# Kernel tuning notes

Measured on AMD Instinct MI355X. Metric: run time of the kernel, lower is better.

Reference implementation:

```python
import jax, jax.numpy as jnp
import numpy as np

DIM = 2048
N_HEADS = 16
KV_RANK = 512
NOPE = 128
ROPE = 64
VDIM = 128
QK_HEAD = NOPE + ROPE  # 192
THETA = 10000.0
EPS = 1e-6
SCALE = QK_HEAD ** -0.5  # mscale == 1.0
NEG_INF = -1e30


def precompute_freqs(seq_len, head_dim, theta=THETA):
    # cos/sin of position*freq, shape (seq_len, head_dim//2)
    freqs = 1.0 / theta ** (np.arange(0, head_dim, 2, dtype=np.float32) / head_dim)
    ang = np.outer(np.arange(seq_len, dtype=np.float32), freqs)
    return jnp.asarray(np.cos(ang)), jnp.asarray(np.sin(ang))


def apply_rope(x, cos, sin):
    # x: (B, S, H, r); cos/sin: (S, r//2). Complex rotation on (even, odd) pairs.
    x2 = x.reshape(*x.shape[:-1], -1, 2)
    x0, x1 = x2[..., 0], x2[..., 1]
    c = cos[None, :, None, :]
    s = sin[None, :, None, :]
    r0 = x0 * c - x1 * s
    r1 = x0 * s + x1 * c
    return jnp.stack([r0, r1], axis=-1).reshape(x.shape)


def rmsnorm(x, w, eps=EPS):
    rms = jnp.sqrt(jnp.mean(x * x, axis=-1, keepdims=True) + eps)
    return x / rms * w


def setup_inputs() -> dict:
    key = jax.random.key(0)
    ks = jax.random.split(key, 5)
    B, S = 2, 2048
    sc = lambda n: 1.0 / np.sqrt(n)
    return {
        "x": jax.random.normal(ks[0], (B, S, DIM), jnp.float32),
        "wq": jax.random.normal(ks[1], (N_HEADS * QK_HEAD, DIM), jnp.float32) * sc(DIM),
        "wkv_a": jax.random.normal(ks[2], (KV_RANK + ROPE, DIM), jnp.float32) * sc(DIM),
        "wkv_b": jax.random.normal(ks[3], (N_HEADS * (NOPE + VDIM), KV_RANK), jnp.float32) * sc(KV_RANK),
        "wo": jax.random.normal(ks[4], (DIM, N_HEADS * VDIM), jnp.float32) * sc(N_HEADS * VDIM),
        "kv_norm_w": jnp.ones((KV_RANK,), jnp.float32),
    }


def reference(x, wq, wkv_a, wkv_b, wo, kv_norm_w):
    # SimpleMLA forward, attn_impl='absorb', start_pos=0 (prefill, causal mask)
    B, S, _ = x.shape
    cos, sin = precompute_freqs(S, ROPE)

    # Q projection (q_lora_rank == 0 -> full rank)
    q = (x @ wq.T).reshape(B, S, N_HEADS, QK_HEAD)
    q_nope, q_pe = q[..., :NOPE], q[..., NOPE:]
    q_pe = apply_rope(q_pe, cos, sin)  # (B,S,H,ROPE)

    # KV-A projection -> latent kv + shared positional key
    kv = x @ wkv_a.T  # (B,S,KV_RANK+ROPE)
    kv_lat, k_pe = kv[..., :KV_RANK], kv[..., KV_RANK:]
    k_pe = apply_rope(k_pe[:, :, None, :], cos, sin)[:, :, 0, :]  # (B,S,ROPE)

    # Absorb: fold wkv_b's nope-half into q; kv_cache is the normalized latent
    wkv_b_h = wkv_b.reshape(N_HEADS, NOPE + VDIM, KV_RANK)
    q_lat = jnp.einsum("bshd,hdc->bshc", q_nope, wkv_b_h[:, :NOPE])  # (B,S,H,C)
    kv_cache = rmsnorm(kv_lat, kv_norm_w)  # (B,T,C)

    scores = (jnp.einsum("bshc,btc->bsht", q_lat, kv_cache)
              + jnp.einsum("bshr,btr->bsht", q_pe, k_pe)) * SCALE
    causal = jnp.tril(jnp.ones((S, S), bool))  # (s, t)
    scores = jnp.where(causal[None, :, None, :], scores, NEG_INF)
    attn = jax.nn.softmax(scores, axis=-1)  # (B,S,H,T)

    out_lat = jnp.einsum("bsht,btc->bshc", attn, kv_cache)  # (B,S,H,C)
    out = jnp.einsum("bshc,hdc->bshd", out_lat, wkv_b_h[:, NOPE:])  # (B,S,H,VDIM)
    return out.reshape(B, S, N_HEADS * VDIM) @ wo.T
```

## Files before the change

kernel.cpp:

```cpp
#include <hip/hip_runtime.h>

typedef unsigned short u16;
typedef unsigned int u32;
typedef __attribute__((ext_vector_type(4))) short short4_t;
typedef __attribute__((ext_vector_type(8))) short short8_t;
typedef __attribute__((ext_vector_type(4))) float f32x4;
typedef __attribute__((ext_vector_type(2))) float f32x2;
typedef __attribute__((ext_vector_type(2))) unsigned int uint2v;
typedef __attribute__((ext_vector_type(8))) __bf16 bf16x8;

#define NH 16
#define SLEN 2048
#define NB 2
#define NTOK 4096
#define SCALE_F 0.07216878364870323f

__device__ __forceinline__ u16 f2bf(float f) {
  unsigned u = __builtin_bit_cast(unsigned, f);
  unsigned r = (u + 0x7FFFu + ((u >> 16) & 1u)) >> 16;
  return (u16)r;
}
__device__ __forceinline__ float bf2f(u16 v) {
  unsigned u = ((unsigned)v) << 16;
  return __builtin_bit_cast(float, u);
}
__device__ __forceinline__ f32x4 mfma16(short8_t a, short8_t b, f32x4 c) {
  return __builtin_amdgcn_mfma_f32_16x16x32_bf16(
      __builtin_bit_cast(bf16x8, a), __builtin_bit_cast(bf16x8, b), c, 0, 0, 0);
}
__device__ __forceinline__ void async16(const u16* g, u16* l) {
  __builtin_amdgcn_global_load_lds(
      (const __attribute__((address_space(1))) unsigned int*)g,
      (__attribute__((address_space(3))) unsigned int*)l, 16, 0, 0);
}

__global__ __launch_bounds__(256) void conv_bf16(const float* __restrict__ in,
                                                 u16* __restrict__ out, int n4) {
  int i = blockIdx.x * 256 + threadIdx.x;
  int stride = gridDim.x * 256;
  for (; i < n4; i += stride) {
    f32x4 v = ((const f32x4*)in)[i];
    short4_t s = {(short)f2bf(v[0]), (short)f2bf(v[1]), (short)f2bf(v[2]),
                  (short)f2bf(v[3])};
    ((short4_t*)out)[i] = s;
  }
}

__global__ void rope_tables(float* __restrict__ cost, float* __restrict__ sint) {
  int s = blockIdx.x, i = threadIdx.x;
  double freq = pow(10000.0, -(double)(2 * i) / 64.0);
  double ang = (double)s * freq;
  cost[s * 32 + i] = (float)cos(ang);
  sint[s * 32 + i] = (float)sin(ang);
}

template <typename TC>
__global__ __launch_bounds__(256) void gemm97(
    const u16* __restrict__ Ag, const u16* __restrict__ Bg, TC* __restrict__ Cg,
    int M, int N, int K, long long sB, long long sC) {
  const u16* A = Ag;
  const u16* B = Bg + (long long)blockIdx.z * sB;
  TC* C = Cg + (long long)blockIdx.z * sC;

  __shared__ u16 As[128 * 32];
  __shared__ u16 Bs[128 * 32];

  const int tid = threadIdx.x;
  const int lane = tid & 63, w = tid >> 6;
  const int l15 = lane & 15, lg = lane >> 4;
  const int wr = (w >> 1) * 64, wc = (w & 1) * 64;
  const int row0 = blockIdx.y * 128, col0 = blockIdx.x * 128;

  const int r0 = tid >> 2;
  const int c0 = (tid & 3) * 8;
  const u16* a0 = A + (long long)(row0 + r0) * K + c0;
  const u16* a1 = A + (long long)(row0 + 64 + r0) * K + c0;
  const int bc0 = min(col0 + r0, N - 1);
  const int bc1 = min(col0 + 64 + r0, N - 1);
  const u16* b0 = B + (long long)bc0 * K + c0;
  const u16* b1 = B + (long long)bc1 * K + c0;

  f32x4 acc[4][4] = {};

  for (int k0 = 0; k0 < K; k0 += 32) {
    __syncthreads();
    async16(a0 + k0, &As[tid * 8]);
    async16(a1 + k0, &As[2048 + tid * 8]);
    async16(b0 + k0, &Bs[tid * 8]);
    async16(b1 + k0, &Bs[2048 + tid * 8]);
    __syncthreads();

    short8_t af[4], bfr[4];
#pragma unroll
    for (int i = 0; i < 4; ++i)
      af[i] = *(const short8_t*)&As[(wr + i * 16 + l15) * 32 + lg * 8];
#pragma unroll
    for (int j = 0; j < 4; ++j)
      bfr[j] = *(const short8_t*)&Bs[(wc + j * 16 + l15) * 32 + lg * 8];
#pragma unroll
    for (int i = 0; i < 4; ++i)
#pragma unroll
      for (int j = 0; j < 4; ++j) acc[i][j] = mfma16(af[i], bfr[j], acc[i][j]);
  }

#pragma unroll
  for (int i = 0; i < 4; ++i)
#pragma unroll
    for (int j = 0; j < 4; ++j)
#pragma unroll
      for (int r = 0; r < 4; ++r) {
        int row = row0 + wr + i * 16 + lg * 4 + r;
        int col = col0 + wc + j * 16 + l15;
        if (col < N) {
          float v = acc[i][j][r];
          if constexpr (sizeof(TC) == 2)
            C[(long long)row * N + col] = (TC)f2bf(v);
          else
            C[(long long)row * N + col] = v;
        }
      }
}

__global__ __launch_bounds__(256) void qprep(
    const u16* __restrict__ qfb, const float* __restrict__ cost,
    const float* __restrict__ sint, u16* __restrict__ qp) {
  int h = blockIdx.y;
  int tok = blockIdx.x * 8 + (threadIdx.x >> 5);
  int l32 = threadIdx.x & 31;
  int b = tok >> 11, s = tok & 2047;
  const u16* src = qfb + (long long)tok * 3072 + h * 192 + 128;
  float x0 = bf2f(src[2 * l32]), x1 = bf2f(src[2 * l32 + 1]);
  float c = cost[s * 32 + l32], sn = sint[s * 32 + l32];
  long long ob = (((long long)(b * NH + h)) * SLEN + s) * 64;
  qp[ob + 2 * l32] = f2bf(x0 * c - x1 * sn);
  qp[ob + 2 * l32 + 1] = f2bf(x0 * sn + x1 * c);
}

__global__ __launch_bounds__(256) void kvprep(
    const float* __restrict__ kvf, const float* __restrict__ wnorm,
    const float* __restrict__ cost, const float* __restrict__ sint,
    u16* __restrict__ kvc, u16* __restrict__ kpe) {
  int r = blockIdx.x;
  int s = r & 2047;
  const float* src = kvf + (long long)r * 576;
  int tid = threadIdx.x;
  f32x2 v = *(const f32x2*)(src + 2 * tid);
  float ss = v[0] * v[0] + v[1] * v[1];
  for (int d = 1; d < 64; d <<= 1) ss += __shfl_xor(ss, d);
  __shared__ float red[4];
  int w = tid >> 6;
  if ((tid & 63) == 0) red[w] = ss;
  __syncthreads();
  float tot = red[0] + red[1] + red[2] + red[3];
  float rinv = 1.0f / sqrtf(tot * (1.0f / 512.0f) + 1e-6f);
  kvc[(long long)r * 512 + 2 * tid] = f2bf(v[0] * rinv * wnorm[2 * tid]);
  kvc[(long long)r * 512 + 2 * tid + 1] = f2bf(v[1] * rinv * wnorm[2 * tid + 1]);
  if (tid < 32) {
    float x0 = src[512 + 2 * tid], x1 = src[512 + 2 * tid + 1];
    float c = cost[s * 32 + tid], sn = sint[s * 32 + tid];
    kpe[(long long)r * 64 + 2 * tid] = f2bf(x0 * c - x1 * sn);
    kpe[(long long)r * 64 + 2 * tid + 1] = f2bf(x0 * sn + x1 * c);
  }
}

__global__ __launch_bounds__(256) void attn_kernel(
    const u16* __restrict__ qfb, const u16* __restrict__ q_pe,
    const u16* __restrict__ knv, const u16* __restrict__ kpe,
    u16* __restrict__ o) {
  const int pairp = blockIdx.x, h = blockIdx.y, b = blockIdx.z;
  const int tid = threadIdx.x, lane = tid & 63, w = tid >> 6;
  const int l15 = lane & 15, lg = lane >> 4;

  __shared__ u16 Kt[64 * 192];
  __shared__ u16 Vt[128][72];
  __shared__ u16 Ps[4][16][72];

  const u16* kvb0 = knv + ((long long)h * NB + b) * (SLEN * 256);
  const u16* kpb0 = kpe + (long long)b * (SLEN * 64);
  const int vq = lane >> 2, vj = lane & 3;

  for (int half = 0; half < 2; ++half) {
    const int qblk = (half == 0) ? pairp : 31 - pairp;
    const int sbase = qblk * 64 + w * 16;

    short8_t qf[6];
    {
      const int srow = sbase + l15;
      const u16* qn = qfb + ((long long)b * SLEN + srow) * 3072 + h * 192;
      const u16* qp = q_pe + (((long long)b * NH + h) * SLEN + srow) * 64;
#pragma unroll
      for (int c = 0; c < 4; ++c) qf[c] = *(const short8_t*)(qn + c * 32 + lg * 8);
#pragma unroll
      for (int c = 0; c < 2; ++c) qf[4 + c] = *(const short8_t*)(qp + c * 32 + lg * 8);
    }

    f32x4 oacc[8] = {};
    float m_run[4], l_run[4];
#pragma unroll
    for (int r = 0; r < 4; ++r) { m_run[r] = -3.0e38f; l_run[r] = 0.f; }

    const int ntiles = qblk + 1;
    const u16* kvb = kvb0;
    const u16* kpb = kpb0;

    for (int tt = 0; tt < ntiles; ++tt) {
      __syncthreads();
#pragma unroll
      for (int it = 0; it < 6; ++it) {
        int p16 = it * 2048 + tid * 8;
        int row = p16 / 192;
        int coll = p16 - row * 192;
        int cols = coll ^ ((row & 7) << 3);
        const u16* src = (cols < 128) ? (kvb + row * 256 + cols)
                                      : (kpb + row * 64 + (cols - 128));
        async16(src, &Kt[p16]);
      }
#pragma unroll
      for (int it = 0; it < 8; ++it) {
        int seg = w * 8 + it;
        int t0 = (seg & 15) << 2;
        int d4 = ((seg >> 4) << 6) + (vq << 2);
        const u16* src = kvb + (t0 + vj) * 256 + 128 + d4;
        uint2v ld = *(const uint2v*)src;
        unsigned A = ld[0], B = ld[1];
        unsigned oA = (unsigned)__shfl_xor((int)A, 1);
        unsigned oB = (unsigned)__shfl_xor((int)B, 1);
        unsigned A1 = (vj & 1) ? ((oA >> 16) | (A & 0xFFFF0000u))
                               : ((A & 0x0000FFFFu) | (oA << 16));
        unsigned B1 = (vj & 1) ? ((oB >> 16) | (B & 0xFFFF0000u))
                               : ((B & 0x0000FFFFu) | (oB << 16));
        unsigned A2 = (unsigned)__shfl_xor((int)A1, 2);
        unsigned B2 = (unsigned)__shfl_xor((int)B1, 2);
        unsigned W0 = (vj & 2) ? B2 : A1;
        unsigned W1 = (vj & 2) ? B1 : A2;
        uint2v wv = {W0, W1};
        *(uint2v*)&Vt[d4 + vj][t0] = wv;
      }
      __syncthreads();

      f32x4 sf[4] = {};
#pragma unroll
      for (int c = 0; c < 6; ++c) {
#pragma unroll
        for (int kt = 0; kt < 4; ++kt) {
          int row = kt * 16 + l15;
          const short8_t kf =
              *(const short8_t*)&Kt[(row * 192 + c * 32 + lg * 8) ^ ((row & 7) << 3)];
          sf[kt] = mfma16(qf[c], kf, sf[kt]);
        }
      }

      const int tb = tt * 64;
      const bool fullt = (tb + 63) <= sbase;
      float p[4][4], mx[4];
#pragma unroll
      for (int r = 0; r < 4; ++r) {
        const int srow = sbase + lg * 4 + r;
        float m = -3.0e38f;
#pragma unroll
        for (int kt = 0; kt < 4; ++kt) {
          const int t = tb + kt * 16 + l15;
          float v = sf[kt][r] * SCALE_F;
          if (!fullt && t > srow) v = -3.0e38f;
          p[r][kt] = v;
          m = fmaxf(m, v);
        }
        mx[r] = m;
      }
#pragma unroll
      for (int d = 1; d < 16; d <<= 1)
#pragma unroll
        for (int r = 0; r < 4; ++r) mx[r] = fmaxf(mx[r], __shfl_xor(mx[r], d));

      float alpha[4];
#pragma unroll
      for (int r = 0; r < 4; ++r) {
        const float mnew = fmaxf(m_run[r], mx[r]);
        alpha[r] = __expf(m_run[r] - mnew);
        float rs = 0.f;
#pragma unroll
        for (int kt = 0; kt < 4; ++kt) {
          const float e = __expf(p[r][kt] - mnew);
          rs += e;
          Ps[w][lg * 4 + r][kt * 16 + l15] = f2bf(e);
        }
#pragma unroll
        for (int d = 1; d < 16; d <<= 1) rs += __shfl_xor(rs, d);
        l_run[r] = l_run[r] * alpha[r] + rs;
        m_run[r] = mnew;
      }
#pragma unroll
      for (int dc = 0; dc < 8; ++dc)
#pragma unroll
        for (int r = 0; r < 4; ++r) oacc[dc][r] *= alpha[r];

      const short8_t pa0 = *(const short8_t*)&Ps[w][l15][lg * 8];
      const short8_t pa1 = *(const short8_t*)&Ps[w][l15][32 + lg * 8];
#pragma unroll
      for (int dc = 0; dc < 8; ++dc) {
        const short8_t v0 = *(const short8_t*)&Vt[dc * 16 + l15][lg * 8];
        const short8_t v1 = *(const short8_t*)&Vt[dc * 16 + l15][32 + lg * 8];
        oacc[dc] = mfma16(pa0, v0, oacc[dc]);
        oacc[dc] = mfma16(pa1, v1, oacc[dc]);
      }
      kvb += 64 * 256;
      kpb += 64 * 64;
    }

    float inv[4];
#pragma unroll
    for (int r = 0; r < 4; ++r) inv[r] = 1.0f / l_run[r];
#pragma unroll
    for (int dc = 0; dc < 8; ++dc)
#pragma unroll
      for (int r = 0; r < 4; ++r) {
        const int srow = sbase + lg * 4 + r;
        o[((long long)b * SLEN + srow) * 2048 + h * 128 + dc * 16 + l15] =
            f2bf(oacc[dc][r] * inv[r]);
      }
  }
}

static const long long OFF_COS   = 0;
static const long long OFF_SIN   = 262144;
static const long long OFF_XB    = 524288;
static const long long OFF_WQB   = 17301504;
static const long long OFF_WKVAB = 29884416;
static const long long OFF_QFB   = 32243712;
static const long long OFF_O     = 524288;
static const long long OFF_KNV   = 57409536;
static const long long OFF_WKVBB = 90963968;
static const long long OFF_WOB   = 95158272;
static const long long OFF_KVF   = 103546880;
static const long long OFF_QP    = 112984064;
static const long long OFF_KVC   = 121372672;
static const long long OFF_KPE   = 125566976;

extern "C" void kernel_launch(void* const* d_in, const int* in_sizes, int n_in,
                              void* d_out, int out_size, void* d_ws, size_t ws_size,
                              hipStream_t stream) {
  const float* x    = (const float*)d_in[0];
  const float* wq   = (const float*)d_in[1];
  const float* wkva = (const float*)d_in[2];
  const float* wkvb = (const float*)d_in[3];
  const float* wo   = (const float*)d_in[4];
  const float* kvnw = (const float*)d_in[5];
  float* out = (float*)d_out;
  char* ws = (char*)d_ws;

  float* cost = (float*)(ws + OFF_COS);
  float* sint = (float*)(ws + OFF_SIN);
  u16* xb    = (u16*)(ws + OFF_XB);
  u16* wqb   = (u16*)(ws + OFF_WQB);
  u16* wkvab = (u16*)(ws + OFF_WKVAB);
  u16* qfb   = (u16*)(ws + OFF_QFB);
  u16* ob    = (u16*)(ws + OFF_O);
  u16* knv   = (u16*)(ws + OFF_KNV);
  u16* wkvbb = (u16*)(ws + OFF_WKVBB);
  u16* wob   = (u16*)(ws + OFF_WOB);
  float* kvf = (float*)(ws + OFF_KVF);
  u16* qp    = (u16*)(ws + OFF_QP);
  u16* kvc   = (u16*)(ws + OFF_KVC);
  u16* kpe   = (u16*)(ws + OFF_KPE);

  rope_tables<<<dim3(SLEN), dim3(32), 0, stream>>>(cost, sint);

  conv_bf16<<<dim3(4096), dim3(256), 0, stream>>>(x, xb, 2097152);
  conv_bf16<<<dim3(4096), dim3(256), 0, stream>>>(wq, wqb, 1572864);
  conv_bf16<<<dim3(1152), dim3(256), 0, stream>>>(wkva, wkvab, 294912);
  conv_bf16<<<dim3(2048), dim3(256), 0, stream>>>(wkvb, wkvbb, 524288);
  conv_bf16<<<dim3(4096), dim3(256), 0, stream>>>(wo, wob, 1048576);

  gemm97<u16><<<dim3(24, 32, 1), dim3(256), 0, stream>>>(
      xb, wqb, qfb, 4096, 3072, 2048, 0LL, 0LL);
  gemm97<float><<<dim3(5, 32, 1), dim3(256), 0, stream>>>(
      xb, wkvab, kvf, 4096, 576, 2048, 0LL, 0LL);

  qprep<<<dim3(512, NH), dim3(256), 0, stream>>>(qfb, cost, sint, qp);
  kvprep<<<dim3(NTOK), dim3(256), 0, stream>>>(kvf, kvnw, cost, sint, kvc, kpe);

  gemm97<u16><<<dim3(2, 32, 16), dim3(256), 0, stream>>>(
      kvc, wkvbb, knv, 4096, 256, 512, (long long)256 * 512,
      (long long)4096 * 256);

  attn_kernel<<<dim3(16, NH, NB), dim3(256), 0, stream>>>(qfb, qp, knv, kpe, ob);

  gemm97<float><<<dim3(16, 32, 1), dim3(256), 0, stream>>>(
      ob, wob, out, 4096, 2048, 2048, 0LL, 0LL);
}
```

Before: 537.7 us.

## Double-buffer attention tiles, pre-transpose V in GEMM, fuse weight conversions

The attention kernel now double-buffers K and V tiles in LDS with async loads, so the next tile is fetched while the current one is computed. It also computes S transposed, so softmax probabilities stay in registers instead of round-tripping through LDS. The K/V projection GEMM writes K and a pre-transposed, pre-permuted V directly, which removes the per-tile shuffle transpose inside attention. The five fp32-to-bf16 conversions are fused into one launch that also folds the softmax scale into wq. Other changes: the rope table launch is reshaped, attention blocks are remapped, s_setprio is used around MFMA sections, and the workspace layout is reorganized with aliasing. The larger LDS footprint and the buffer aliasing add occupancy and correctness risk.

```diff
diff --git a/kernel.cpp b/kernel.cpp
--- a/kernel.cpp
+++ b/kernel.cpp
@@ -7,6 +7,7 @@
 typedef __attribute__((ext_vector_type(4))) float f32x4;
 typedef __attribute__((ext_vector_type(2))) float f32x2;
 typedef __attribute__((ext_vector_type(2))) unsigned int uint2v;
+typedef __attribute__((ext_vector_type(4))) unsigned int uint4v;
 typedef __attribute__((ext_vector_type(8))) __bf16 bf16x8;
 
 #define NH 16
@@ -24,6 +25,11 @@
   unsigned u = ((unsigned)v) << 16;
   return __builtin_bit_cast(float, u);
 }
+__device__ __forceinline__ u32 cvtpk(float a, float b) {
+  u32 d;
+  asm("v_cvt_pk_bf16_f32 %0, %1, %2" : "=v"(d) : "v"(a), "v"(b));
+  return d;
+}
 __device__ __forceinline__ f32x4 mfma16(short8_t a, short8_t b, f32x4 c) {
   return __builtin_amdgcn_mfma_f32_16x16x32_bf16(
       __builtin_bit_cast(bf16x8, a), __builtin_bit_cast(bf16x8, b), c, 0, 0, 0);
@@ -34,20 +40,34 @@
       (__attribute__((address_space(3))) unsigned int*)l, 16, 0, 0);
 }
 
-__global__ __launch_bounds__(256) void conv_bf16(const float* __restrict__ in,
-                                                 u16* __restrict__ out, int n4) {
+__global__ __launch_bounds__(256) void convall(
+    const float* __restrict__ x, const float* __restrict__ wq,
+    const float* __restrict__ wkva, const float* __restrict__ wkvb,
+    const float* __restrict__ wo, u16* __restrict__ xb, u16* __restrict__ wqb,
+    u16* __restrict__ wkvab, u16* __restrict__ wkvbb, u16* __restrict__ wob) {
   int i = blockIdx.x * 256 + threadIdx.x;
-  int stride = gridDim.x * 256;
-  for (; i < n4; i += stride) {
-    f32x4 v = ((const f32x4*)in)[i];
-    short4_t s = {(short)f2bf(v[0]), (short)f2bf(v[1]), (short)f2bf(v[2]),
-                  (short)f2bf(v[3])};
-    ((short4_t*)out)[i] = s;
-  }
-}
-
-__global__ void rope_tables(float* __restrict__ cost, float* __restrict__ sint) {
-  int s = blockIdx.x, i = threadIdx.x;
+  const int stride = gridDim.x * 256;
+  for (; i < 5537792; i += stride) {
+    const float* src;
+    u16* dst;
+    int j;
+    float sc = 1.0f;
+    if (i < 2097152) { src = x; dst = xb; j = i; }
+    else if (i < 3670016) { src = wq; dst = wqb; j = i - 2097152; sc = SCALE_F; }
+    else if (i < 3964928) { src = wkva; dst = wkvab; j = i - 3670016; }
+    else if (i < 4489216) { src = wkvb; dst = wkvbb; j = i - 3964928; }
+    else { src = wo; dst = wob; j = i - 4489216; }
+    f32x4 v = ((const f32x4*)src)[j];
+    short4_t s = {(short)f2bf(v[0] * sc), (short)f2bf(v[1] * sc),
+                  (short)f2bf(v[2] * sc), (short)f2bf(v[3] * sc)};
+    ((short4_t*)dst)[j] = s;
+  }
+}
+
+__global__ __launch_bounds__(256) void rope_tables(float* __restrict__ cost,
+                                                   float* __restrict__ sint) {
+  int s = blockIdx.x * 8 + (threadIdx.x >> 5);
+  int i = threadIdx.x & 31;
   double freq = pow(10000.0, -(double)(2 * i) / 64.0);
   double ang = (double)s * freq;
   cost[s * 32 + i] = (float)cos(ang);
@@ -119,6 +139,79 @@
             C[(long long)row * N + col] = v;
         }
       }
+}
+
+__global__ __launch_bounds__(256) void gemm_knv(
+    const u16* __restrict__ A, const u16* __restrict__ Bg,
+    u16* __restrict__ kn, u16* __restrict__ vtb) {
+  const int z = blockIdx.z;
+  const u16* B = Bg + (long long)z * (256 * 512);
+
+  __shared__ u16 As[128 * 32];
+  __shared__ u16 Bs[128 * 32];
+
+  const int tid = threadIdx.x;
+  const int lane = tid & 63, w = tid >> 6;
+  const int l15 = lane & 15, lg = lane >> 4;
+  const int wr = (w >> 1) * 64, wc = (w & 1) * 64;
+  const int row0 = blockIdx.y * 128, col0 = blockIdx.x * 128;
+  const int K = 512;
+
+  const int r0 = tid >> 2;
+  const int c0 = (tid & 3) * 8;
+  const u16* a0 = A + (long long)(row0 + r0) * K + c0;
+  const u16* a1 = A + (long long)(row0 + 64 + r0) * K + c0;
+  const u16* b0 = B + (long long)(col0 + r0) * K + c0;
+  const u16* b1 = B + (long long)(col0 + 64 + r0) * K + c0;
+
+  f32x4 acc[4][4] = {};
+
+  for (int k0 = 0; k0 < K; k0 += 32) {
+    __syncthreads();
+    async16(a0 + k0, &As[tid * 8]);
+    async16(a1 + k0, &As[2048 + tid * 8]);
+    async16(b0 + k0, &Bs[tid * 8]);
+    async16(b1 + k0, &Bs[2048 + tid * 8]);
+    __syncthreads();
+
+    short8_t af[4], bfr[4];
+#pragma unroll
+    for (int i = 0; i < 4; ++i)
+      af[i] = *(const short8_t*)&As[(wr + i * 16 + l15) * 32 + lg * 8];
+#pragma unroll
+    for (int j = 0; j < 4; ++j)
+      bfr[j] = *(const short8_t*)&Bs[(wc + j * 16 + l15) * 32 + lg * 8];
+#pragma unroll
+    for (int i = 0; i < 4; ++i)
+#pragma unroll
+      for (int j = 0; j < 4; ++j) acc[i][j] = mfma16(af[i], bfr[j], acc[i][j]);
+  }
+
+  if (col0 == 0) {
+    u16* Ck = kn + (long long)z * 4096 * 128;
+#pragma unroll
+    for (int i = 0; i < 4; ++i)
+#pragma unroll
+      for (int j = 0; j < 4; ++j)
+#pragma unroll
+        for (int r = 0; r < 4; ++r) {
+          int row = row0 + wr + i * 16 + lg * 4 + r;
+          int col = wc + j * 16 + l15;
+          Ck[(long long)row * 128 + col] = f2bf(acc[i][j][r]);
+        }
+  } else {
+#pragma unroll
+    for (int i = 0; i < 4; ++i)
+#pragma unroll
+      for (int j = 0; j < 4; ++j) {
+        int d = wc + j * 16 + l15;
+        int row = row0 + wr + i * 16 + lg * 4;
+        int kpos = (row & ~31) | (((row >> 2) & 3) << 3) | (((row >> 4) & 1) << 2);
+        uint2v pk = {cvtpk(acc[i][j][0], acc[i][j][1]),
+                     cvtpk(acc[i][j][2], acc[i][j][3])};
+        *(uint2v*)(vtb + (long long)(z * 128 + d) * 4096 + kpos) = pk;
+      }
+  }
 }
 
 __global__ __launch_bounds__(256) void qprep(
@@ -165,158 +258,174 @@
 
 __global__ __launch_bounds__(256) void attn_kernel(
     const u16* __restrict__ qfb, const u16* __restrict__ q_pe,
-    const u16* __restrict__ knv, const u16* __restrict__ kpe,
-    u16* __restrict__ o) {
-  const int pairp = blockIdx.x, h = blockIdx.y, b = blockIdx.z;
+    const u16* __restrict__ kn, const u16* __restrict__ vt,
+    const u16* __restrict__ kpe, u16* __restrict__ o) {
+  const int bid = blockIdx.x;
+  const int lp = (bid & 7) * 64 + (bid >> 3);
+  const int pairp = lp & 15, h = (lp >> 4) & 15, b = lp >> 8;
   const int tid = threadIdx.x, lane = tid & 63, w = tid >> 6;
   const int l15 = lane & 15, lg = lane >> 4;
 
-  __shared__ u16 Kt[64 * 192];
-  __shared__ u16 Vt[128][72];
-  __shared__ u16 Ps[4][16][72];
-
-  const u16* kvb0 = knv + ((long long)h * NB + b) * (SLEN * 256);
-  const u16* kpb0 = kpe + (long long)b * (SLEN * 64);
-  const int vq = lane >> 2, vj = lane & 3;
+  __shared__ u16 KT[2][64 * 192];
+  __shared__ u16 VTl[2][64 * 128];
+
+  const u16* knp = kn + ((long long)h * 4096 + b * 2048) * 128;
+  const u16* kpb = kpe + (long long)b * 2048 * 64;
+  const u16* vtp = vt + (long long)h * 128 * 4096 + b * 2048;
+
+  const int sw = (l15 & 7) << 4;
+  const int voff0 = ((lg * 16) ^ sw) >> 1;
+  const int voff1 = ((64 + lg * 16) ^ sw) >> 1;
 
   for (int half = 0; half < 2; ++half) {
     const int qblk = (half == 0) ? pairp : 31 - pairp;
     const int sbase = qblk * 64 + w * 16;
+    const int srow = sbase + l15;
 
     short8_t qf[6];
     {
-      const int srow = sbase + l15;
-      const u16* qn = qfb + ((long long)b * SLEN + srow) * 3072 + h * 192;
-      const u16* qp = q_pe + (((long long)b * NH + h) * SLEN + srow) * 64;
+      const u16* qn = qfb + ((long long)b * 2048 + srow) * 3072 + h * 192;
+      const u16* qp = q_pe + (((long long)b * 16 + h) * 2048 + srow) * 64;
 #pragma unroll
       for (int c = 0; c < 4; ++c) qf[c] = *(const short8_t*)(qn + c * 32 + lg * 8);
 #pragma unroll
       for (int c = 0; c < 2; ++c) qf[4 + c] = *(const short8_t*)(qp + c * 32 + lg * 8);
     }
 
+    const u16* srcK[6];
+    int bumpK[6];
+#pragma unroll
+    for (int it = 0; it < 6; ++it) {
+      int p16 = it * 2048 + tid * 8;
+      int row = p16 / 192;
+      int coll = p16 - row * 192;
+      int cols = coll ^ ((row & 7) << 3);
+      if (cols < 128) { srcK[it] = knp + row * 128 + cols; bumpK[it] = 64 * 128; }
+      else            { srcK[it] = kpb + row * 64 + (cols - 128); bumpK[it] = 64 * 64; }
+    }
+    const u16* srcV[4];
+#pragma unroll
+    for (int it = 0; it < 4; ++it) {
+      int dp = it * 4096 + tid * 16;
+      int d = dp >> 7;
+      int t = ((dp & 127) ^ ((d & 7) << 4)) >> 1;
+      srcV[it] = vtp + (long long)d * 4096 + t;
+    }
+
     f32x4 oacc[8] = {};
-    float m_run[4], l_run[4];
-#pragma unroll
-    for (int r = 0; r < 4; ++r) { m_run[r] = -3.0e38f; l_run[r] = 0.f; }
-
+    float m_run = -3.0e38f, l_run = 0.f;
     const int ntiles = qblk + 1;
-    const u16* kvb = kvb0;
-    const u16* kpb = kpb0;
+
+    auto STAGE = [&](int bi) {
+      u16* kd = &KT[bi][tid * 8];
+      u16* vd = &VTl[bi][tid * 8];
+#pragma unroll
+      for (int it = 0; it < 6; ++it) async16(srcK[it], kd + it * 2048);
+#pragma unroll
+      for (int it = 0; it < 4; ++it) async16(srcV[it], vd + it * 2048);
+#pragma unroll
+      for (int it = 0; it < 6; ++it) srcK[it] += bumpK[it];
+#pragma unroll
+      for (int it = 0; it < 4; ++it) srcV[it] += 64;
+    };
+
+    __syncthreads();
+    STAGE(0);
+    int cur = 0;
 
     for (int tt = 0; tt < ntiles; ++tt) {
       __syncthreads();
-#pragma unroll
-      for (int it = 0; it < 6; ++it) {
-        int p16 = it * 2048 + tid * 8;
-        int row = p16 / 192;
-        int coll = p16 - row * 192;
-        int cols = coll ^ ((row & 7) << 3);
-        const u16* src = (cols < 128) ? (kvb + row * 256 + cols)
-                                      : (kpb + row * 64 + (cols - 128));
-        async16(src, &Kt[p16]);
-      }
-#pragma unroll
-      for (int it = 0; it < 8; ++it) {
-        int seg = w * 8 + it;
-        int t0 = (seg & 15) << 2;
-        int d4 = ((seg >> 4) << 6) + (vq << 2);
-        const u16* src = kvb + (t0 + vj) * 256 + 128 + d4;
-        uint2v ld = *(const uint2v*)src;
-        unsigned A = ld[0], B = ld[1];
-        unsigned oA = (unsigned)__shfl_xor((int)A, 1);
-        unsigned oB = (unsigned)__shfl_xor((int)B, 1);
-        unsigned A1 = (vj & 1) ? ((oA >> 16) | (A & 0xFFFF0000u))
-                               : ((A & 0x0000FFFFu) | (oA << 16));
-        unsigned B1 = (vj & 1) ? ((oB >> 16) | (B & 0xFFFF0000u))
-                               : ((B & 0x0000FFFFu) | (oB << 16));
-        unsigned A2 = (unsigned)__shfl_xor((int)A1, 2);
-        unsigned B2 = (unsigned)__shfl_xor((int)B1, 2);
-        unsigned W0 = (vj & 2) ? B2 : A1;
-        unsigned W1 = (vj & 2) ? B1 : A2;
-        uint2v wv = {W0, W1};
-        *(uint2v*)&Vt[d4 + vj][t0] = wv;
-      }
-      __syncthreads();
-
+      if (tt + 1 < ntiles) STAGE(cur ^ 1);
+
+      const u16* Kc = &KT[cur][0];
       f32x4 sf[4] = {};
+      __builtin_amdgcn_s_setprio(1);
 #pragma unroll
       for (int c = 0; c < 6; ++c) {
 #pragma unroll
-        for (int kt = 0; kt < 4; ++kt) {
-          int row = kt * 16 + l15;
+        for (int i = 0; i < 4; ++i) {
+          int row = i * 16 + l15;
           const short8_t kf =
-              *(const short8_t*)&Kt[(row * 192 + c * 32 + lg * 8) ^ ((row & 7) << 3)];
-          sf[kt] = mfma16(qf[c], kf, sf[kt]);
+              *(const short8_t*)&Kc[(row * 192 + c * 32 + lg * 8) ^ ((row & 7) << 3)];
+          sf[i] = mfma16(kf, qf[c], sf[i]);
         }
       }
+      __builtin_amdgcn_s_setprio(0);
 
       const int tb = tt * 64;
-      const bool fullt = (tb + 63) <= sbase;
-      float p[4][4], mx[4];
-#pragma unroll
-      for (int r = 0; r < 4; ++r) {
-        const int srow = sbase + lg * 4 + r;
-        float m = -3.0e38f;
-#pragma unroll
-        for (int kt = 0; kt < 4; ++kt) {
-          const int t = tb + kt * 16 + l15;
-          float v = sf[kt][r] * SCALE_F;
-          if (!fullt && t > srow) v = -3.0e38f;
-          p[r][kt] = v;
-          m = fmaxf(m, v);
+      if (!((tb + 63) <= sbase)) {
+#pragma unroll
+        for (int i = 0; i < 4; ++i)
+#pragma unroll
+          for (int r = 0; r < 4; ++r) {
+            int t = tb + i * 16 + lg * 4 + r;
+            if (t > srow) sf[i][r] = -3.0e38f;
+          }
+      }
+
+      float mx = sf[0][0];
+#pragma unroll
+      for (int i = 0; i < 4; ++i)
+#pragma unroll
+        for (int r = 0; r < 4; ++r) mx = fmaxf(mx, sf[i][r]);
+      mx = fmaxf(mx, __shfl_xor(mx, 16));
+      mx = fmaxf(mx, __shfl_xor(mx, 32));
+      const float mnew = fmaxf(m_run, mx);
+      const float alpha = __expf(m_run - mnew);
+      float ev[4][4];
+      float rs = 0.f;
+#pragma unroll
+      for (int i = 0; i < 4; ++i)
+#pragma unroll
+        for (int r = 0; r < 4; ++r) {
+          float e = __expf(sf[i][r] - mnew);
+          ev[i][r] = e;
+          rs += e;
         }
-        mx[r] = m;
-      }
-#pragma unroll
-      for (int d = 1; d < 16; d <<= 1)
-#pragma unroll
-        for (int r = 0; r < 4; ++r) mx[r] = fmaxf(mx[r], __shfl_xor(mx[r], d));
-
-      float alpha[4];
-#pragma unroll
-      for (int r = 0; r < 4; ++r) {
-        const float mnew = fmaxf(m_run[r], mx[r]);
-        alpha[r] = __expf(m_run[r] - mnew);
-        float rs = 0.f;
-#pragma unroll
-        for (int kt = 0; kt < 4; ++kt) {
-          const float e = __expf(p[r][kt] - mnew);
-          rs += e;
-          Ps[w][lg * 4 + r][kt * 16 + l15] = f2bf(e);
-        }
-#pragma unroll
-        for (int d = 1; d < 16; d <<= 1) rs += __shfl_xor(rs, d);
-        l_run[r] = l_run[r] * alpha[r] + rs;
-        m_run[r] = mnew;
-      }
+      rs += __shfl_xor(rs, 16);
+      rs += __shfl_xor(rs, 32);
+      l_run = l_run * alpha + rs;
+      m_run = mnew;
+
+      float alphaq[4];
+#pragma unroll
+      for (int r = 0; r < 4; ++r) alphaq[r] = __shfl(alpha, lg * 4 + r);
 #pragma unroll
       for (int dc = 0; dc < 8; ++dc)
 #pragma unroll
-        for (int r = 0; r < 4; ++r) oacc[dc][r] *= alpha[r];
-
-      const short8_t pa0 = *(const short8_t*)&Ps[w][l15][lg * 8];
-      const short8_t pa1 = *(const short8_t*)&Ps[w][l15][32 + lg * 8];
+        for (int r = 0; r < 4; ++r) oacc[dc][r] *= alphaq[r];
+
+      uint4v u0 = {cvtpk(ev[0][0], ev[0][1]), cvtpk(ev[0][2], ev[0][3]),
+                   cvtpk(ev[1][0], ev[1][1]), cvtpk(ev[1][2], ev[1][3])};
+      uint4v u1 = {cvtpk(ev[2][0], ev[2][1]), cvtpk(ev[2][2], ev[2][3]),
+                   cvtpk(ev[3][0], ev[3][1]), cvtpk(ev[3][2], ev[3][3])};
+      const short8_t pa0 = __builtin_bit_cast(short8_t, u0);
+      const short8_t pa1 = __builtin_bit_cast(short8_t, u1);
+
+      const u16* Vc = &VTl[cur][0];
+      __builtin_amdgcn_s_setprio(1);
 #pragma unroll
       for (int dc = 0; dc < 8; ++dc) {
-        const short8_t v0 = *(const short8_t*)&Vt[dc * 16 + l15][lg * 8];
-        const short8_t v1 = *(const short8_t*)&Vt[dc * 16 + l15][32 + lg * 8];
+        const int rbase = (dc * 16 + l15) * 64;
+        const short8_t v0 = *(const short8_t*)&Vc[rbase + voff0];
+        const short8_t v1 = *(const short8_t*)&Vc[rbase + voff1];
         oacc[dc] = mfma16(pa0, v0, oacc[dc]);
         oacc[dc] = mfma16(pa1, v1, oacc[dc]);
       }
-      kvb += 64 * 256;
-      kpb += 64 * 64;
+      __builtin_amdgcn_s_setprio(0);
+      cur ^= 1;
     }
 
-    float inv[4];
-#pragma unroll
-    for (int r = 0; r < 4; ++r) inv[r] = 1.0f / l_run[r];
+    float invq[4];
+#pragma unroll
+    for (int r = 0; r < 4; ++r) invq[r] = 1.0f / __shfl(l_run, lg * 4 + r);
 #pragma unroll
     for (int dc = 0; dc < 8; ++dc)
 #pragma unroll
       for (int r = 0; r < 4; ++r) {
-        const int srow = sbase + lg * 4 + r;
-        o[((long long)b * SLEN + srow) * 2048 + h * 128 + dc * 16 + l15] =
-            f2bf(oacc[dc][r] * inv[r]);
+        const int sr = sbase + lg * 4 + r;
+        o[((long long)b * 2048 + sr) * 2048 + h * 128 + dc * 16 + l15] =
+            f2bf(oacc[dc][r] * invq[r]);
       }
   }
 }
@@ -326,15 +435,15 @@
 static const long long OFF_XB    = 524288;
 static const long long OFF_WQB   = 17301504;
 static const long long OFF_WKVAB = 29884416;
-static const long long OFF_QFB   = 32243712;
-static const long long OFF_O     = 524288;
-static const long long OFF_KNV   = 57409536;
-static const long long OFF_WKVBB = 90963968;
-static const long long OFF_WOB   = 95158272;
-static const long long OFF_KVF   = 103546880;
-static const long long OFF_QP    = 112984064;
-static const long long OFF_KVC   = 121372672;
-static const long long OFF_KPE   = 125566976;
+static const long long OFF_KVF   = 32243712;
+static const long long OFF_KN    = 17301504;
+static const long long OFF_QFB   = 41680896;
+static const long long OFF_VT    = 66846720;
+static const long long OFF_WKVBB = 83623936;
+static const long long OFF_KVC   = 87818240;
+static const long long OFF_KPE   = 92012544;
+static const long long OFF_QP    = 92536832;
+static const long long OFF_WOB   = 100925440;
 
 extern "C" void kernel_launch(void* const* d_in, const int* in_sizes, int n_in,
                               void* d_out, int out_size, void* d_ws, size_t ws_size,
@@ -351,25 +460,22 @@
   float* cost = (float*)(ws + OFF_COS);
   float* sint = (float*)(ws + OFF_SIN);
   u16* xb    = (u16*)(ws + OFF_XB);
+  u16* ob    = (u16*)(ws + OFF_XB);
   u16* wqb   = (u16*)(ws + OFF_WQB);
   u16* wkvab = (u16*)(ws + OFF_WKVAB);
+  float* kvf = (float*)(ws + OFF_KVF);
+  u16* kn    = (u16*)(ws + OFF_KN);
   u16* qfb   = (u16*)(ws + OFF_QFB);
-  u16* ob    = (u16*)(ws + OFF_O);
-  u16* knv   = (u16*)(ws + OFF_KNV);
+  u16* vt    = (u16*)(ws + OFF_VT);
   u16* wkvbb = (u16*)(ws + OFF_WKVBB);
-  u16* wob   = (u16*)(ws + OFF_WOB);
-  float* kvf = (float*)(ws + OFF_KVF);
-  u16* qp    = (u16*)(ws + OFF_QP);
   u16* kvc   = (u16*)(ws + OFF_KVC);
   u16* kpe   = (u16*)(ws + OFF_KPE);
-
-  rope_tables<<<dim3(SLEN), dim3(32), 0, stream>>>(cost, sint);
-
-  conv_bf16<<<dim3(4096), dim3(256), 0, stream>>>(x, xb, 2097152);
-  conv_bf16<<<dim3(4096), dim3(256), 0, stream>>>(wq, wqb, 1572864);
-  conv_bf16<<<dim3(1152), dim3(256), 0, stream>>>(wkva, wkvab, 294912);
-  conv_bf16<<<dim3(2048), dim3(256), 0, stream>>>(wkvb, wkvbb, 524288);
-  conv_bf16<<<dim3(4096), dim3(256), 0, stream>>>(wo, wob, 1048576);
+  u16* qp    = (u16*)(ws + OFF_QP);
+  u16* wob   = (u16*)(ws + OFF_WOB);
+
+  rope_tables<<<dim3(256), dim3(256), 0, stream>>>(cost, sint);
+  convall<<<dim3(2048), dim3(256), 0, stream>>>(x, wq, wkva, wkvb, wo, xb, wqb,
+                                                wkvab, wkvbb, wob);
 
   gemm97<u16><<<dim3(24, 32, 1), dim3(256), 0, stream>>>(
       xb, wqb, qfb, 4096, 3072, 2048, 0LL, 0LL);
@@ -379,11 +485,9 @@
   qprep<<<dim3(512, NH), dim3(256), 0, stream>>>(qfb, cost, sint, qp);
   kvprep<<<dim3(NTOK), dim3(256), 0, stream>>>(kvf, kvnw, cost, sint, kvc, kpe);
 
-  gemm97<u16><<<dim3(2, 32, 16), dim3(256), 0, stream>>>(
-      kvc, wkvbb, knv, 4096, 256, 512, (long long)256 * 512,
-      (long long)4096 * 256);
-
-  attn_kernel<<<dim3(16, NH, NB), dim3(256), 0, stream>>>(qfb, qp, knv, kpe, ob);
+  gemm_knv<<<dim3(2, 32, 16), dim3(256), 0, stream>>>(kvc, wkvbb, kn, vt);
+
+  attn_kernel<<<dim3(512), dim3(256), 0, stream>>>(qfb, qp, kn, vt, kpe, ob);
 
   gemm97<float><<<dim3(16, 32, 1), dim3(256), 0, stream>>>(
       ob, wob, out, 4096, 2048, 2048, 0LL, 0LL);
```

Result: faster. 458.9 us (-14.6%).
